# Kernel tuning notes

Measured on AMD Instinct MI355X. Metric: run time of the kernel, lower is better.

## Reference

```python
import jax, jax.numpy as jnp
import numpy as np

DIM = 512; NHEAD = 8; DHEAD = 64; INNER = NHEAD * DHEAD
CTX = 1024; NOCT = int(np.ceil(np.log2(CTX))) + 1  # 11
B = 8; SEQ = 256; MEM = 768


def positional_encoding(ctx, num_oct):
    # matches Attention.positional_encoding on coords=arange(ctx).view(ctx,1),
    # start_octave = 1 - num_oct
    coords = jnp.arange(ctx, dtype=jnp.float32)[:, None, None]        # (ctx,1,1)
    octaves = jnp.arange(1 - num_oct, 1, dtype=jnp.float32)           # (num_oct,)
    mult = (2.0 ** octaves) * np.pi
    scaled = (coords * mult).reshape(ctx, num_oct)                    # (ctx, num_oct)
    return jnp.concatenate([jnp.sin(scaled), jnp.cos(scaled)], axis=-1)  # (ctx, 2*num_oct)


def get_shifts(mem, seq, ctx):
    coords = jnp.arange(mem + seq - 1, -1, -1) - (seq - 1)            # (mem+seq,)
    shifts = coords[None, :] + jnp.arange(seq)[:, None]               # (seq, mem+seq)
    oob = (shifts < 0) | (shifts > ctx - 1)
    bias = jnp.where(oob, -jnp.inf, 0.0).astype(jnp.float32)
    return jnp.clip(shifts, 0, ctx - 1), bias


def setup_inputs() -> dict:
    key = jax.random.key(0)
    ks = jax.random.split(key, 8)
    s = 0.02
    return {
        "x": jax.random.normal(ks[0], (B, SEQ, DIM), jnp.float32),
        "memory": jax.random.normal(ks[1], (B, MEM, DIM), jnp.float32),
        "W_qkv": jax.random.normal(ks[2], (DIM, 3 * INNER), jnp.float32) * s,
        "W_rel": jax.random.normal(ks[3], (2 * NOCT, INNER), jnp.float32) * s,
        "W_out": jax.random.normal(ks[4], (INNER, DIM), jnp.float32) * s,
        "b_out": jnp.zeros((DIM,), jnp.float32),
        "u_emb": jax.random.normal(ks[5], (DHEAD,), jnp.float32),
        "v_emb": jax.random.normal(ks[6], (DHEAD,), jnp.float32),
    }


def reference(x, memory, W_qkv, W_rel, W_out, b_out, u_emb, v_emb):
    b, seq, _ = x.shape
    mem = memory.shape[1]
    total = mem + seq
    scale = DHEAD ** -0.5

    shifts, bias = get_shifts(mem, seq, CTX)                          # (seq,total) each
    R = positional_encoding(CTX, NOCT)                                # (CTX, 2*NOCT)
    kr = (R @ W_rel)[shifts].reshape(seq, total, NHEAD, DHEAD)        # n m h d

    qkv = jnp.concatenate([memory, x], axis=1) @ W_qkv                # (b,total,3*INNER)
    q, k, v = jnp.split(qkv, 3, axis=-1)

    def heads(t):
        return t.reshape(b, total, NHEAD, DHEAD).transpose(0, 2, 1, 3)  # b h m d

    q = heads(q)[:, :, mem:]                                          # b h n d (queries only over x)
    k = heads(k)
    v = heads(v)

    term_a = jnp.einsum('bhnd,bhmd->bhnm', q, k)
    term_b = jnp.einsum('bhnd,nmhd->bhnm', q, kr)
    term_c = jnp.einsum('d,bhmd->bhm', u_emb, k)[:, :, None, :]        # broadcast over n
    term_d = jnp.einsum('d,nmhd->hnm', v_emb, kr)[None]                # broadcast over b

    dots = (term_a + term_b + term_c + term_d) * scale + bias          # banded -inf mask
    attn = jax.nn.softmax(dots, axis=-1)                               # dropout p=0 -> identity
    out = jnp.einsum('bhnm,bhmd->bnhd', attn, v).reshape(b, seq, INNER)
    return out @ W_out + b_out
```

## Files before the change

### kernel.cpp

```cpp
#include <hip/hip_runtime.h>
#include <hip/hip_bf16.h>
#include <math.h>

typedef unsigned short u16;
typedef unsigned int u32;
typedef __attribute__((ext_vector_type(8))) short short8;
typedef __attribute__((ext_vector_type(4))) float floatx4;

constexpr int kB     = 8;
constexpr int kSEQ   = 256;
constexpr int kMEM   = 768;
constexpr int kTOTAL = 1024;

__device__ __forceinline__ float bf2f(u16 u) {
  return __uint_as_float(((u32)u) << 16);
}
__device__ __forceinline__ u16 f2bf(float f) {
  __hip_bfloat16 h = __float2bfloat16(f);
  return *reinterpret_cast<u16*>(&h);
}
__device__ __forceinline__ void gload_lds16(const u16* g, u16* l) {
  __builtin_amdgcn_global_load_lds(
      (__attribute__((address_space(1))) const unsigned int*)g,
      (__attribute__((address_space(3))) unsigned int*)l, 16, 0, 0);
}

__device__ __forceinline__ void wtconv_body(
    const float* __restrict__ W, u16* __restrict__ Wt, int K, int N,
    int n0, int k0, int tid, float (*tile)[65])
{
  int r = tid >> 4, c4 = (tid & 15) * 4;
#pragma unroll
  for (int v = 0; v < 4; v++) {
    float4 w4 = *(const float4*)(W + (size_t)(k0 + v * 16 + r) * N + n0 + c4);
    tile[v * 16 + r][c4 + 0] = w4.x;
    tile[v * 16 + r][c4 + 1] = w4.y;
    tile[v * 16 + r][c4 + 2] = w4.z;
    tile[v * 16 + r][c4 + 3] = w4.w;
  }
  __syncthreads();
#pragma unroll
  for (int v = 0; v < 4; v++) {
    int rn = v * 16 + r;
    ushort4 o;
    o.x = f2bf(tile[c4 + 0][rn]);
    o.y = f2bf(tile[c4 + 1][rn]);
    o.z = f2bf(tile[c4 + 2][rn]);
    o.w = f2bf(tile[c4 + 3][rn]);
    *(ushort4*)(Wt + (size_t)(n0 + rn) * K + k0 + c4) = o;
  }
}

__global__ __launch_bounds__(256) void prep_kernel(
    const float* __restrict__ x, const float* __restrict__ memf,
    const float* __restrict__ W_qkv, const float* __restrict__ W_out,
    const float* __restrict__ W_rel, const float* __restrict__ v_emb,
    const float* __restrict__ u_emb,
    u16* __restrict__ Xb, u16* __restrict__ WqkvT, u16* __restrict__ WoutT,
    u16* __restrict__ Rrel_bf, float* __restrict__ vR, u16* __restrict__ u_bf)
{
  __shared__ float tile[64][65];
  __shared__ float pe[22];
  __shared__ float prod[512];
  int bid = blockIdx.x;
  int t = threadIdx.x;
  if (bid < 1024) {
    int s = bid;
    if (bid == 0 && t >= 128 && t < 192) {
      u_bf[t - 128] = f2bf(0.125f * u_emb[t - 128]);
    }
    if (t < 22) {
      int o = (t < 11) ? t : (t - 11);
      float mult = ldexpf(3.14159265358979323846f, o - 10);
      float ang = (float)s * mult;
      pe[t] = (t < 11) ? sinf(ang) : cosf(ang);
    }
    __syncthreads();
#pragma unroll
    for (int c = 0; c < 2; c++) {
      int j = t + c * 256;
      float acc = 0.f;
#pragma unroll
      for (int o = 0; o < 22; ++o) acc += pe[o] * W_rel[o * 512 + j];
      Rrel_bf[(size_t)s * 512 + j] = f2bf(acc);
      prod[j] = acc * v_emb[j & 63];
    }
    __syncthreads();
    if (t < 8) {
      float a = 0.f;
#pragma unroll 8
      for (int d = 0; d < 64; d++) a += prod[t * 64 + d];
      vR[t * 1024 + s] = a * 0.125f;
    }
  } else if (bid < 3072) {
    int idx = (bid - 1024) * 256 + t;
    int row = idx >> 6, c8 = idx & 63;
    int b = row >> 10, pos = row & 1023;
    const float* src = (pos < kMEM)
        ? memf + (size_t)(b * kMEM + pos) * 512
        : x    + (size_t)(b * kSEQ + pos - kMEM) * 512;
    const float4* s4 = (const float4*)(src + c8 * 8);
    float4 a = s4[0], bb = s4[1];
    u16 tmp[8] = {f2bf(a.x),  f2bf(a.y),  f2bf(a.z),  f2bf(a.w),
                  f2bf(bb.x), f2bf(bb.y), f2bf(bb.z), f2bf(bb.w)};
    *(uint4*)(Xb + (size_t)row * 512 + c8 * 8) = *(uint4*)tmp;
  } else if (bid < 3264) {
    int r = bid - 3072;
    wtconv_body(W_qkv, WqkvT, 512, 1536, (r % 24) * 64, (r / 24) * 64, t, tile);
  } else {
    int r = bid - 3264;
    wtconv_body(W_out, WoutT, 512, 512, (r % 8) * 64, (r / 8) * 64, t, tile);
  }
}

__global__ __launch_bounds__(256) void gemm_bf16(
    const u16* __restrict__ A, const u16* __restrict__ Bt,
    int lda, int ldb, int ksteps,
    u16* __restrict__ Cbf, int ldc, int qscale)
{
  __shared__ u16 As[128 * 64];
  __shared__ u16 Bs[128 * 64];
  int tid = threadIdx.x;
  int id = blockIdx.y * gridDim.x + blockIdx.x;
  int gy = gridDim.y;
  int bm = (id % gy) * 128, bn = (id / gy) * 128;
  int ln = tid & 15, quad = (tid >> 4) & 3, w = tid >> 6;
  int moff = (w >> 1) * 64, noff = (w & 1) * 64;
  int l7 = ln & 7;
  floatx4 acc[4][4];
#pragma unroll
  for (int mi = 0; mi < 4; mi++)
#pragma unroll
    for (int ni = 0; ni < 4; ni++) acc[mi][ni] = (floatx4){0.f, 0.f, 0.f, 0.f};

  int srow[4], sgch[4];
#pragma unroll
  for (int v = 0; v < 4; v++) {
    int f = v * 256 + tid;
    srow[v] = f >> 3;
    sgch[v] = (f & 7) ^ ((f >> 3) & 7);
  }

  for (int ks = 0; ks < ksteps; ks++) {
    int k0 = ks * 64;
#pragma unroll
    for (int v = 0; v < 4; v++) {
      gload_lds16(A + (size_t)(bm + srow[v]) * lda + k0 + sgch[v] * 8,
                  &As[(v * 256 + tid) * 8]);
      gload_lds16(Bt + (size_t)(bn + srow[v]) * ldb + k0 + sgch[v] * 8,
                  &Bs[(v * 256 + tid) * 8]);
    }
    __syncthreads();
#pragma unroll
    for (int kb = 0; kb < 2; kb++) {
      short8 af[4], bfr[4];
#pragma unroll
      for (int mi = 0; mi < 4; mi++) {
        int row = moff + mi * 16 + ln;
        af[mi] = *(const short8*)&As[row * 64 + (((quad + 4 * kb) ^ l7) << 3)];
      }
#pragma unroll
      for (int ni = 0; ni < 4; ni++) {
        int row = noff + ni * 16 + ln;
        bfr[ni] = *(const short8*)&Bs[row * 64 + (((quad + 4 * kb) ^ l7) << 3)];
      }
#pragma unroll
      for (int mi = 0; mi < 4; mi++)
#pragma unroll
        for (int ni = 0; ni < 4; ni++)
          acc[mi][ni] = __builtin_amdgcn_mfma_f32_16x16x32_bf16(
              af[mi], bfr[ni], acc[mi][ni], 0, 0, 0);
    }
    __syncthreads();
  }

  int r0 = bm + moff + quad * 4;
#pragma unroll
  for (int ni = 0; ni < 4; ni++) {
    int col = bn + noff + ni * 16 + ln;
    float scale = (qscale && col < 512) ? 0.125f : 1.f;
#pragma unroll
    for (int mi = 0; mi < 4; mi++) {
#pragma unroll
      for (int r = 0; r < 4; r++) {
        int row = r0 + mi * 16 + r;
        Cbf[(size_t)row * ldc + col] = f2bf(acc[mi][ni][r] * scale);
      }
    }
  }
}

__global__ __launch_bounds__(256) void gemm_bf16_64(
    const u16* __restrict__ A, const u16* __restrict__ Bt,
    int lda, int ldb, int ksteps,
    float* __restrict__ Cf, int ldc, const float* __restrict__ bias)
{
  __shared__ u16 As[64 * 64];
  __shared__ u16 Bs[64 * 64];
  int tid = threadIdx.x;
  int id = blockIdx.y * gridDim.x + blockIdx.x;
  int gy = gridDim.y;
  int bm = (id % gy) * 64, bn = (id / gy) * 64;
  int ln = tid & 15, quad = (tid >> 4) & 3, w = tid >> 6;
  int moff = (w >> 1) * 32, noff = (w & 1) * 32;
  int l7 = ln & 7;
  floatx4 acc[2][2];
#pragma unroll
  for (int mi = 0; mi < 2; mi++)
#pragma unroll
    for (int ni = 0; ni < 2; ni++) acc[mi][ni] = (floatx4){0.f, 0.f, 0.f, 0.f};

  int srow[2], sgch[2];
#pragma unroll
  for (int v = 0; v < 2; v++) {
    int f = v * 256 + tid;
    srow[v] = f >> 3;
    sgch[v] = (f & 7) ^ ((f >> 3) & 7);
  }

  for (int ks = 0; ks < ksteps; ks++) {
    int k0 = ks * 64;
#pragma unroll
    for (int v = 0; v < 2; v++) {
      gload_lds16(A + (size_t)(bm + srow[v]) * lda + k0 + sgch[v] * 8,
                  &As[(v * 256 + tid) * 8]);
      gload_lds16(Bt + (size_t)(bn + srow[v]) * ldb + k0 + sgch[v] * 8,
                  &Bs[(v * 256 + tid) * 8]);
    }
    __syncthreads();
#pragma unroll
    for (int kb = 0; kb < 2; kb++) {
      short8 af[2], bfr[2];
#pragma unroll
      for (int mi = 0; mi < 2; mi++) {
        int row = moff + mi * 16 + ln;
        af[mi] = *(const short8*)&As[row * 64 + (((quad + 4 * kb) ^ l7) << 3)];
      }
#pragma unroll
      for (int ni = 0; ni < 2; ni++) {
        int row = noff + ni * 16 + ln;
        bfr[ni] = *(const short8*)&Bs[row * 64 + (((quad + 4 * kb) ^ l7) << 3)];
      }
#pragma unroll
      for (int mi = 0; mi < 2; mi++)
#pragma unroll
        for (int ni = 0; ni < 2; ni++)
          acc[mi][ni] = __builtin_amdgcn_mfma_f32_16x16x32_bf16(
              af[mi], bfr[ni], acc[mi][ni], 0, 0, 0);
    }
    __syncthreads();
  }

  int r0 = bm + moff + quad * 4;
#pragma unroll
  for (int ni = 0; ni < 2; ni++) {
    int col = bn + noff + ni * 16 + ln;
    float cv = bias[col];
#pragma unroll
    for (int mi = 0; mi < 2; mi++) {
#pragma unroll
      for (int r = 0; r < 4; r++) {
        int row = r0 + mi * 16 + r;
        Cf[(size_t)row * ldc + col] = acc[mi][ni][r] + cv;
      }
    }
  }
}

__global__ __launch_bounds__(256) void attn_mfma(
    const u16* __restrict__ qkv_bf, const u16* __restrict__ Rrel_bf,
    const float* __restrict__ vR, const u16* __restrict__ u_bf,
    u16* __restrict__ Opart, float* __restrict__ lbuf)
{
  constexpr int LD = 72;
  __shared__ u16 Vt[2][64 * LD];
  __shared__ u16 Ps[64 * LD];

  int nt = blockIdx.x >> 3, p = blockIdx.x & 7;
  int h = blockIdx.y, b = blockIdx.z;
  int n0 = nt * 64, bh = b * 8 + h;
  int tid = threadIdx.x;
  int w = tid >> 6, lane = tid & 63;
  int l15 = lane & 15, quad = lane >> 4, q8 = quad * 8;

  int sr0 = tid >> 3, sc8 = tid & 7;
  int sr1 = (256 + tid) >> 3;
  int vg0 = ((sr0 >> 3) ^ sc8) * 8 + (sr0 & 7);
  int vg1 = ((sr1 >> 3) ^ sc8) * 8 + (sr1 & 7);

  const u16* qrow = qkv_bf + (size_t)(b * kTOTAL + kMEM + n0 + 16 * w + l15) * 1536 + h * 64;
  short8 qf0 = *(const short8*)(qrow + q8);
  short8 qf1 = *(const short8*)(qrow + 32 + q8);

  int bidx[4];
#pragma unroll
  for (int r = 0; r < 4; r++) {
    int il = 4 * quad + r;
    bidx[r] = ((quad << 4) | ((il + 15 - l15) & 15)) << 2;
  }

  const u16* kpart = qkv_bf + (size_t)(b * kTOTAL) * 1536 + 512 + h * 64;
  const float* vRh = vR + h * 1024;

  int ntiles = 13 + nt;
  int mtA = p, mtB = p + 8;
  bool hasB = (mtB < ntiles);
  bool lastB = (mtB == ntiles - 1);

  {
    const u16* va = kpart + (size_t)mtA * 64 * 1536 + 512;
    const u16* vb = kpart + (size_t)mtB * 64 * 1536 + 512;
    uint4 a0 = *(const uint4*)(va + (size_t)sr0 * 1536 + sc8 * 8);
    uint4 a1 = *(const uint4*)(va + (size_t)sr1 * 1536 + sc8 * 8);
    uint4 b0 = *(const uint4*)(vb + (size_t)sr0 * 1536 + sc8 * 8);
    uint4 b1 = *(const uint4*)(vb + (size_t)sr1 * 1536 + sc8 * 8);
    const u16* pa0v = (const u16*)&a0;
    const u16* pa1v = (const u16*)&a1;
    const u16* pb0v = (const u16*)&b0;
    const u16* pb1v = (const u16*)&b1;
#pragma unroll
    for (int i = 0; i < 8; i++) {
      Vt[0][(sc8 * 8 + i) * LD + vg0] = pa0v[i];
      Vt[0][(sc8 * 8 + i) * LD + vg1] = pa1v[i];
      Vt[1][(sc8 * 8 + i) * LD + vg0] = pb0v[i];
      Vt[1][(sc8 * 8 + i) * LD + vg1] = pb1v[i];
    }
  }
  __syncthreads();

  floatx4 o_acc[4];
  float l_i[4];
#pragma unroll
  for (int r = 0; r < 4; r++) l_i[r] = 0.f;
#pragma unroll
  for (int nd = 0; nd < 4; nd++) o_acc[nd] = (floatx4){0.f, 0.f, 0.f, 0.f};

  int s_base_w = kMEM + n0 + 16 * w;

  auto tile_body = [&](int mt, bool lastt, const u16* VtX) {
    int m0 = mt * 64;
    const u16* kbase = kpart + (size_t)m0 * 1536;
    int sb = s_base_w - m0;

    short8 kb0[4], kb1[4];
#pragma unroll
    for (int ni = 0; ni < 4; ni++) {
      const u16* kr = kbase + (size_t)(16 * ni + l15) * 1536;
      kb0[ni] = *(const short8*)(kr + q8);
      kb1[ni] = *(const short8*)(kr + 32 + q8);
    }

    float uk[4];
    {
      short8 uf0 = *(const short8*)(u_bf + q8);
      short8 uf1 = *(const short8*)(u_bf + 32 + q8);
#pragma unroll
      for (int ni = 0; ni < 4; ni++) {
        floatx4 ua = (floatx4){0.f, 0.f, 0.f, 0.f};
        ua = __builtin_amdgcn_mfma_f32_16x16x32_bf16(uf0, kb0[ni], ua, 0, 0, 0);
        ua = __builtin_amdgcn_mfma_f32_16x16x32_bf16(uf1, kb1[ni], ua, 0, 0, 0);
        uk[ni] = ua[0];
      }
    }

    float tf[5][4];
#pragma unroll
    for (int ct = 0; ct < 5; ct++) {
      int s = sb - 63 + 16 * ct + l15;
      s = min(max(s, 0), 1023);
      const u16* rr = Rrel_bf + (size_t)s * 512 + h * 64;
      short8 rb0 = *(const short8*)(rr + q8);
      short8 rb1 = *(const short8*)(rr + 32 + q8);
      float vv = vRh[s];
      floatx4 t = (floatx4){0.f, 0.f, 0.f, 0.f};
      t = __builtin_amdgcn_mfma_f32_16x16x32_bf16(qf0, rb0, t, 0, 0, 0);
      t = __builtin_amdgcn_mfma_f32_16x16x32_bf16(qf1, rb1, t, 0, 0, 0);
#pragma unroll
      for (int r = 0; r < 4; r++) tf[ct][r] = t[r] + vv;
    }

#pragma unroll
    for (int ni = 0; ni < 4; ni++) {
      floatx4 sa = (floatx4){0.f, 0.f, 0.f, 0.f};
      sa = __builtin_amdgcn_mfma_f32_16x16x32_bf16(qf0, kb0[ni], sa, 0, 0, 0);
      sa = __builtin_amdgcn_mfma_f32_16x16x32_bf16(qf1, kb1[ni], sa, 0, 0, 0);
#pragma unroll
      for (int r = 0; r < 4; r++) {
        int il = 4 * quad + r;
        float tv = (l15 < il) ? tf[4 - ni][r] : tf[3 - ni][r];
        float tsh = __int_as_float(
            __builtin_amdgcn_ds_bpermute(bidx[r], __float_as_int(tv)));
        float val = sa[r] + tsh + uk[ni];
        if (lastt && (16 * ni + l15) > (16 * w + il)) val = -1e30f;
        float e = __expf(val);
        l_i[r] += e;
        int prow = 16 * w + il;
        Ps[prow * LD + (l15 & 7) + (((2 * ni + (l15 >> 3)) ^ (prow >> 3)) << 3)] =
            f2bf(e);
      }
    }

    int rowq = 16 * w + l15, rr3q = rowq >> 3;
    short8 pa0 = *(const short8*)&Ps[rowq * LD + ((quad ^ rr3q) << 3)];
    short8 pa1 = *(const short8*)&Ps[rowq * LD + (((quad + 4) ^ rr3q) << 3)];
#pragma unroll
    for (int nd = 0; nd < 4; nd++) {
      int rowv = 16 * nd + l15, rr3v = rowv >> 3;
      short8 vb0 = *(const short8*)&VtX[rowv * LD + ((quad ^ rr3v) << 3)];
      short8 vb1 = *(const short8*)&VtX[rowv * LD + (((quad + 4) ^ rr3v) << 3)];
      o_acc[nd] = __builtin_amdgcn_mfma_f32_16x16x32_bf16(pa0, vb0, o_acc[nd], 0, 0, 0);
      o_acc[nd] = __builtin_amdgcn_mfma_f32_16x16x32_bf16(pa1, vb1, o_acc[nd], 0, 0, 0);
    }
  };

  tile_body(mtA, false, Vt[0]);
  if (hasB) tile_body(mtB, lastB, Vt[1]);

  int pbase = (p * 64 + bh) * 256;
#pragma unroll
  for (int r = 0; r < 4; r++) {
    float l = l_i[r];
#pragma unroll
    for (int off = 1; off < 16; off <<= 1)
      l += __shfl_xor(l, off, 64);
    int n = n0 + 16 * w + 4 * quad + r;
    u16* orow = Opart + ((size_t)(pbase + n) << 6) + l15;
#pragma unroll
    for (int nd = 0; nd < 4; nd++)
      orow[16 * nd] = f2bf(o_acc[nd][r]);
    if (l15 == 0) lbuf[pbase + n] = l;
  }
}

__global__ __launch_bounds__(256) void attn_combine(
    const u16* __restrict__ Opart, const float* __restrict__ lbuf,
    u16* __restrict__ aout_bf)
{
  int idx = blockIdx.x * 256 + threadIdx.x;
  int bh = idx >> 12, n = (idx >> 4) & 255, d4 = idx & 15;
  int rowi = bh * 256 + n;
  float den = 0.f;
  float num[4] = {0.f, 0.f, 0.f, 0.f};
#pragma unroll
  for (int p = 0; p < 8; p++) {
    den += lbuf[(p << 14) + rowi];
    uint2 raw = *(const uint2*)(Opart + (((size_t)(p << 14) + rowi) << 6) + d4 * 4);
    const u16* us = (const u16*)&raw;
#pragma unroll
    for (int j = 0; j < 4; j++) num[j] += bf2f(us[j]);
  }
  float inv = 1.f / den;
  int b = bh >> 3, h = bh & 7;
  ushort4 o;
  o.x = f2bf(num[0] * inv);
  o.y = f2bf(num[1] * inv);
  o.z = f2bf(num[2] * inv);
  o.w = f2bf(num[3] * inv);
  *(ushort4*)(aout_bf + (size_t)(b * kSEQ + n) * 512 + h * 64 + d4 * 4) = o;
}

extern "C" void kernel_launch(void* const* d_in, const int* in_sizes, int n_in,
                              void* d_out, int out_size, void* d_ws, size_t ws_size,
                              hipStream_t stream) {
  (void)in_sizes; (void)n_in; (void)out_size; (void)ws_size;
  const float* x      = (const float*)d_in[0];
  const float* memory = (const float*)d_in[1];
  const float* W_qkv  = (const float*)d_in[2];
  const float* W_rel  = (const float*)d_in[3];
  const float* W_out  = (const float*)d_in[4];
  const float* b_out  = (const float*)d_in[5];
  const float* u_emb  = (const float*)d_in[6];
  const float* v_emb  = (const float*)d_in[7];
  float* out = (float*)d_out;

  char* ws = (char*)d_ws;
  u16*   qkv_bf  = (u16*)ws;                         ws += (size_t)12582912 * 2;
  u16*   Xcat_bf = (u16*)ws;                         ws += (size_t)4194304 * 2;
  u16*   aout_bf = (u16*)ws;                         ws += (size_t)1048576 * 2;
  u16*   Opart   = (u16*)ws;                         ws += (size_t)8388608 * 2;
  float* lbuf    = (float*)ws;                       ws += (size_t)131072 * 4;
  u16*   WqkvT   = (u16*)ws;                         ws += (size_t)786432 * 2;
  u16*   WoutT   = (u16*)ws;                         ws += (size_t)262144 * 2;
  u16*   Rrel_bf = (u16*)ws;                         ws += (size_t)524288 * 2;
  float* vR      = (float*)ws;                       ws += (size_t)8192 * 4;
  u16*   u_bf    = (u16*)ws;                         ws += (size_t)128;

  prep_kernel<<<3328, 256, 0, stream>>>(
      x, memory, W_qkv, W_out, W_rel, v_emb, u_emb,
      Xcat_bf, WqkvT, WoutT, Rrel_bf, vR, u_bf);

  gemm_bf16<<<dim3(12, 64), 256, 0, stream>>>(
      Xcat_bf, WqkvT, 512, 512, 8, qkv_bf, 1536, 1);

  attn_mfma<<<dim3(32, 8, 8), 256, 0, stream>>>(
      qkv_bf, Rrel_bf, vR, u_bf, Opart, lbuf);

  attn_combine<<<1024, 256, 0, stream>>>(Opart, lbuf, aout_bf);

  gemm_bf16_64<<<dim3(8, 32), 256, 0, stream>>>(
      aout_bf, WoutT, 512, 512, 8, out, 512, b_out);
}
```

Measured before the change: 166.5 us.

## Fold u-bias into query projection and correct positional term algebraically

```diff
diff --git a/kernel.cpp b/kernel.cpp
--- a/kernel.cpp
+++ b/kernel.cpp
@@ -57,7 +57,7 @@
     const float* __restrict__ W_rel, const float* __restrict__ v_emb,
     const float* __restrict__ u_emb,
     u16* __restrict__ Xb, u16* __restrict__ WqkvT, u16* __restrict__ WoutT,
-    u16* __restrict__ Rrel_bf, float* __restrict__ vR, u16* __restrict__ u_bf)
+    u16* __restrict__ Rrel_bf, float* __restrict__ vR)
 {
   __shared__ float tile[64][65];
   __shared__ float pe[22];
@@ -66,9 +66,6 @@
   int t = threadIdx.x;
   if (bid < 1024) {
     int s = bid;
-    if (bid == 0 && t >= 128 && t < 192) {
-      u_bf[t - 128] = f2bf(0.125f * u_emb[t - 128]);
-    }
     if (t < 22) {
       int o = (t < 11) ? t : (t - 11);
       float mult = ldexpf(3.14159265358979323846f, o - 10);
@@ -82,8 +79,9 @@
       float acc = 0.f;
 #pragma unroll
       for (int o = 0; o < 22; ++o) acc += pe[o] * W_rel[o * 512 + j];
-      Rrel_bf[(size_t)s * 512 + j] = f2bf(acc);
-      prod[j] = acc * v_emb[j & 63];
+      u16 rbf = f2bf(acc);
+      Rrel_bf[(size_t)s * 512 + j] = rbf;
+      prod[j] = acc * v_emb[j & 63] - bf2f(rbf) * u_emb[j & 63];
     }
     __syncthreads();
     if (t < 8) {
@@ -116,7 +114,7 @@
 __global__ __launch_bounds__(256) void gemm_bf16(
     const u16* __restrict__ A, const u16* __restrict__ Bt,
     int lda, int ldb, int ksteps,
-    u16* __restrict__ Cbf, int ldc, int qscale)
+    u16* __restrict__ Cbf, int ldc, int qscale, const float* __restrict__ uq)
 {
   __shared__ u16 As[128 * 64];
   __shared__ u16 Bs[128 * 64];
@@ -178,13 +176,15 @@
 #pragma unroll
   for (int ni = 0; ni < 4; ni++) {
     int col = bn + noff + ni * 16 + ln;
-    float scale = (qscale && col < 512) ? 0.125f : 1.f;
+    bool isq = qscale && col < 512;
+    float scale = isq ? 0.125f : 1.f;
+    float uadd = isq ? uq[col & 63] : 0.f;
 #pragma unroll
     for (int mi = 0; mi < 4; mi++) {
 #pragma unroll
       for (int r = 0; r < 4; r++) {
         int row = r0 + mi * 16 + r;
-        Cbf[(size_t)row * ldc + col] = f2bf(acc[mi][ni][r] * scale);
+        Cbf[(size_t)row * ldc + col] = f2bf((acc[mi][ni][r] + uadd) * scale);
       }
     }
   }
@@ -269,7 +269,7 @@
 
 __global__ __launch_bounds__(256) void attn_mfma(
     const u16* __restrict__ qkv_bf, const u16* __restrict__ Rrel_bf,
-    const float* __restrict__ vR, const u16* __restrict__ u_bf,
+    const float* __restrict__ vR,
     u16* __restrict__ Opart, float* __restrict__ lbuf)
 {
   constexpr int LD = 72;
@@ -350,19 +350,6 @@
       kb1[ni] = *(const short8*)(kr + 32 + q8);
     }
 
-    float uk[4];
-    {
-      short8 uf0 = *(const short8*)(u_bf + q8);
-      short8 uf1 = *(const short8*)(u_bf + 32 + q8);
-#pragma unroll
-      for (int ni = 0; ni < 4; ni++) {
-        floatx4 ua = (floatx4){0.f, 0.f, 0.f, 0.f};
-        ua = __builtin_amdgcn_mfma_f32_16x16x32_bf16(uf0, kb0[ni], ua, 0, 0, 0);
-        ua = __builtin_amdgcn_mfma_f32_16x16x32_bf16(uf1, kb1[ni], ua, 0, 0, 0);
-        uk[ni] = ua[0];
-      }
-    }
-
     float tf[5][4];
 #pragma unroll
     for (int ct = 0; ct < 5; ct++) {
@@ -379,18 +366,33 @@
       for (int r = 0; r < 4; r++) tf[ct][r] = t[r] + vv;
     }
 
+    float tsh[4][4];
 #pragma unroll
     for (int ni = 0; ni < 4; ni++) {
-      floatx4 sa = (floatx4){0.f, 0.f, 0.f, 0.f};
-      sa = __builtin_amdgcn_mfma_f32_16x16x32_bf16(qf0, kb0[ni], sa, 0, 0, 0);
-      sa = __builtin_amdgcn_mfma_f32_16x16x32_bf16(qf1, kb1[ni], sa, 0, 0, 0);
 #pragma unroll
       for (int r = 0; r < 4; r++) {
         int il = 4 * quad + r;
         float tv = (l15 < il) ? tf[4 - ni][r] : tf[3 - ni][r];
-        float tsh = __int_as_float(
+        tsh[ni][r] = __int_as_float(
             __builtin_amdgcn_ds_bpermute(bidx[r], __float_as_int(tv)));
-        float val = sa[r] + tsh + uk[ni];
+      }
+    }
+
+    floatx4 sa[4];
+#pragma unroll
+    for (int ni = 0; ni < 4; ni++) {
+      floatx4 s4 = (floatx4){0.f, 0.f, 0.f, 0.f};
+      s4 = __builtin_amdgcn_mfma_f32_16x16x32_bf16(qf0, kb0[ni], s4, 0, 0, 0);
+      s4 = __builtin_amdgcn_mfma_f32_16x16x32_bf16(qf1, kb1[ni], s4, 0, 0, 0);
+      sa[ni] = s4;
+    }
+
+#pragma unroll
+    for (int ni = 0; ni < 4; ni++) {
+#pragma unroll
+      for (int r = 0; r < 4; r++) {
+        int il = 4 * quad + r;
+        float val = sa[ni][r] + tsh[ni][r];
         if (lastt && (16 * ni + l15) > (16 * w + il)) val = -1e30f;
         float e = __expf(val);
         l_i[r] += e;
@@ -483,17 +485,16 @@
   u16*   WoutT   = (u16*)ws;                         ws += (size_t)262144 * 2;
   u16*   Rrel_bf = (u16*)ws;                         ws += (size_t)524288 * 2;
   float* vR      = (float*)ws;                       ws += (size_t)8192 * 4;
-  u16*   u_bf    = (u16*)ws;                         ws += (size_t)128;
 
   prep_kernel<<<3328, 256, 0, stream>>>(
       x, memory, W_qkv, W_out, W_rel, v_emb, u_emb,
-      Xcat_bf, WqkvT, WoutT, Rrel_bf, vR, u_bf);
+      Xcat_bf, WqkvT, WoutT, Rrel_bf, vR);
 
   gemm_bf16<<<dim3(12, 64), 256, 0, stream>>>(
-      Xcat_bf, WqkvT, 512, 512, 8, qkv_bf, 1536, 1);
+      Xcat_bf, WqkvT, 512, 512, 8, qkv_bf, 1536, 1, u_emb);
 
   attn_mfma<<<dim3(32, 8, 8), 256, 0, stream>>>(
-      qkv_bf, Rrel_bf, vR, u_bf, Opart, lbuf);
+      qkv_bf, Rrel_bf, vR, Opart, lbuf);
 
   attn_combine<<<1024, 256, 0, stream>>>(Opart, lbuf, aout_bf);
 
```

New measurement: 157.7 us. 5.3% less time.
